# Kernel tuning notes

Hardware: AMD Instinct MI355X
Metric: run time of the kernel (lower is better)

## Reference

```python
import jax, jax.numpy as jnp
import numpy as np

N_NODES = 50000

def setup_inputs() -> dict:
    key = jax.random.key(0)
    k1, k2, k3, k4, k5 = jax.random.split(key, 5)
    x = jax.random.normal(k1, (50000, 64), dtype=jnp.float32)
    adj_rows = jax.random.randint(k2, (800000,), 0, 50000, dtype=jnp.int32)
    adj_cols = jax.random.randint(k3, (800000,), 0, 50000, dtype=jnp.int32)
    adj_vals = jax.random.uniform(k4, (800000,), dtype=jnp.float32)
    ws = jax.random.uniform(k5, (4,), dtype=jnp.float32)
    return {"x": x, "adj_rows": adj_rows, "adj_cols": adj_cols, "adj_vals": adj_vals, "ws": ws, "idx": 0}

def reference(x, adj_rows, adj_cols, adj_vals, ws, idx):
    # spmm: out[r] = sum_{e: rows[e]==r} vals[e] * x[cols[e]]
    msgs = adj_vals[:, None] * x[adj_cols]              # [E, d]
    spmm = jax.ops.segment_sum(msgs, adj_rows, num_segments=N_NODES)  # [N, d]
    return ws[idx] * spmm
```

## Files before the change

kernel.cpp:

```cpp
#include <hip/hip_runtime.h>

#define N_NODES 50000
#define N_EDGES 800000
#define D 64

#define NBUCK 782
#define CAP   2048
#define SRT_CAP 2048

#define A_EPB 4096
#define A_BLOCKS ((N_EDGES + A_EPB - 1) / A_EPB)
#define A_THREADS 512

#define F_THREADS 512

typedef unsigned short ushort_t;

__global__ __launch_bounds__(256) void cvt_kernel(
    const float* __restrict__ x, ushort_t* __restrict__ xb,
    int* __restrict__ gcur)
{
    if (blockIdx.x == 0) {
        for (int j = threadIdx.x; j < NBUCK; j += 256) gcur[j] = j * CAP;
    }
    int i = blockIdx.x * 256 + threadIdx.x;
    float4 v = reinterpret_cast<const float4*>(x)[i];
    ushort4 o;
    unsigned bx;
    bx = __float_as_uint(v.x); o.x = (ushort_t)((bx + 0x7fffu + ((bx >> 16) & 1u)) >> 16);
    bx = __float_as_uint(v.y); o.y = (ushort_t)((bx + 0x7fffu + ((bx >> 16) & 1u)) >> 16);
    bx = __float_as_uint(v.z); o.z = (ushort_t)((bx + 0x7fffu + ((bx >> 16) & 1u)) >> 16);
    bx = __float_as_uint(v.w); o.w = (ushort_t)((bx + 0x7fffu + ((bx >> 16) & 1u)) >> 16);
    reinterpret_cast<ushort4*>(xb)[i] = o;
}

__global__ __launch_bounds__(A_THREADS) void bin_kernel(
    const int* __restrict__ rows, const int* __restrict__ cols,
    const float* __restrict__ vals, int* __restrict__ gcur,
    int2* __restrict__ buckets)
{
    __shared__ int2 rec[A_EPB];
    __shared__ int2 srt[A_EPB];
    __shared__ int cnt[NBUCK];
    __shared__ int lofs[NBUCK];
    __shared__ int lcur[NBUCK];
    __shared__ int bbase[NBUCK];

    const int tid = threadIdx.x;
    const int e0  = blockIdx.x * A_EPB;
    const int n   = min(A_EPB, N_EDGES - e0);

    for (int i = tid; i < NBUCK; i += A_THREADS) cnt[i] = 0;
    __syncthreads();

    for (int i = tid; i < n; i += A_THREADS) {
        int r = rows[e0 + i];
        int c = cols[e0 + i];
        float v = vals[e0 + i];
        rec[i].x = (int)(((unsigned)r << 16) | (unsigned)c);
        rec[i].y = __float_as_int(v);
        atomicAdd(&cnt[r >> 6], 1);
    }
    __syncthreads();

    if (tid < 64) {
        int lane = tid, carry = 0;
        for (int seg = 0; seg < (NBUCK + 63) / 64; ++seg) {
            int j = seg * 64 + lane;
            int v = (j < NBUCK) ? cnt[j] : 0;
            int incl = v;
            for (int off = 1; off < 64; off <<= 1) {
                int u = __shfl_up(incl, off);
                if (lane >= off) incl += u;
            }
            if (j < NBUCK) lofs[j] = carry + incl - v;
            carry += __shfl(incl, 63);
        }
    }
    __syncthreads();

    for (int j = tid; j < NBUCK; j += A_THREADS) {
        int c = cnt[j];
        bbase[j] = c ? atomicAdd(&gcur[j], c) : 0;
        lcur[j]  = lofs[j];
    }
    __syncthreads();

    for (int i = tid; i < n; i += A_THREADS) {
        int2 rv = rec[i];
        int b = ((unsigned)rv.x) >> 22;
        int p = atomicAdd(&lcur[b], 1);
        srt[p] = rv;
    }
    __syncthreads();

    for (int i = tid; i < n; i += A_THREADS) {
        int2 rv = srt[i];
        int b = ((unsigned)rv.x) >> 22;
        buckets[bbase[b] + (i - lofs[b])] = rv;
    }
}

__global__ __launch_bounds__(F_THREADS) void sortgather_kernel(
    const ushort_t* __restrict__ xb, const int2* __restrict__ buckets,
    const int* __restrict__ gcur, const float* __restrict__ ws,
    const int* __restrict__ idx, float* __restrict__ out)
{
    __shared__ int2 srt[SRT_CAP];
    __shared__ int cnt[64];
    __shared__ int lofs[65];
    __shared__ int lcur[64];

    const int b    = blockIdx.x;
    const int tid  = threadIdx.x;
    const int lane = tid & 63;
    const int w    = tid >> 6;
    const int base = b * CAP;
    const int nb   = gcur[b] - base;

    if (tid < 64) cnt[tid] = 0;
    __syncthreads();

    for (int i = tid; i < nb; i += F_THREADS) {
        int rx = buckets[base + i].x;
        atomicAdd(&cnt[(rx >> 16) & 63], 1);
    }
    __syncthreads();

    if (w == 0) {
        int v = cnt[lane];
        int incl = v;
        for (int off = 1; off < 64; off <<= 1) {
            int u = __shfl_up(incl, off);
            if (lane >= off) incl += u;
        }
        lofs[lane] = incl - v;
        if (lane == 63) lofs[64] = incl;
    }
    __syncthreads();
    if (tid < 64) lcur[tid] = lofs[tid];
    __syncthreads();

    for (int i = tid; i < nb; i += F_THREADS) {
        int2 rv = buckets[base + i];
        int p = atomicAdd(&lcur[(rv.x >> 16) & 63], 1);
        srt[p] = make_int2((rv.x & 0xffff) << 7, rv.y);
    }
    __syncthreads();

    const float wgt = ws[idx[0]];
    const int g4       = (lane >> 5) << 2;
    const int lane_off = (lane & 31) << 2;
    const char* xbase  = (const char*)xb;

    for (int q = 0; q < 8; ++q) {
        const int lr = w * 8 + q;
        const int s0 = lofs[lr];
        const int s1 = lofs[lr + 1];
        float accL = 0.f, accH = 0.f;
        for (int cb = s0; cb < s1; cb += 32) {
            int le = cb + (lane & 31);
            int2 cv = srt[le < s1 ? le : s0];
            int offs  = cv.x;
            int vbits = (le < s1) ? cv.y : 0;
#pragma unroll
            for (int p = 0; p < 16; ++p) {
                int src = g4 + (p << 3);
                int o  = __builtin_amdgcn_ds_bpermute(src, offs);
                int vb = __builtin_amdgcn_ds_bpermute(src, vbits);
                unsigned u2 = *reinterpret_cast<const unsigned*>(
                    xbase + (unsigned)o + lane_off);
                float xlo = __uint_as_float(u2 << 16);
                float xhi = __uint_as_float(u2 & 0xffff0000u);
                float v = __int_as_float(vb);
                if (p & 1) { accH += v * xhi; accL += v * xlo; }
                else       { accL += v * xlo; accH += v * xhi; }
            }
        }
        accL += __shfl_xor(accL, 32);
        accH += __shfl_xor(accH, 32);
        const int row = b * 64 + lr;
        if (lane < 32 && row < N_NODES) {
            float2 o2 = make_float2(wgt * accL, wgt * accH);
            reinterpret_cast<float2*>(out)[(size_t)row * (D / 2) + (lane & 31)] = o2;
        }
    }
}

extern "C" void kernel_launch(void* const* d_in, const int* in_sizes, int n_in,
                              void* d_out, int out_size, void* d_ws, size_t ws_size,
                              hipStream_t stream) {
    const float* x    = (const float*)d_in[0];
    const int*   rows = (const int*)d_in[1];
    const int*   cols = (const int*)d_in[2];
    const float* vals = (const float*)d_in[3];
    const float* ws   = (const float*)d_in[4];
    const int*   idx  = (const int*)d_in[5];
    float*       out  = (float*)d_out;

    const size_t xb_bytes      = (size_t)N_NODES * D * sizeof(ushort_t);
    const size_t buckets_bytes = (size_t)NBUCK * CAP * sizeof(int2);

    char* wsb = (char*)d_ws;
    ushort_t* xb      = (ushort_t*)wsb;
    int2*     buckets = (int2*)(wsb + xb_bytes);
    int*      gcur    = (int*)(wsb + xb_bytes + buckets_bytes);

    cvt_kernel<<<dim3(N_NODES * D / 4 / 256), dim3(256), 0, stream>>>(x, xb, gcur);

    bin_kernel<<<dim3(A_BLOCKS), dim3(A_THREADS), 0, stream>>>(
        rows, cols, vals, gcur, buckets);

    sortgather_kernel<<<dim3(NBUCK), dim3(F_THREADS), 0, stream>>>(
        xb, buckets, gcur, ws, idx, out);
}
```

Baseline: 55.66 us.

## Halve bucket size to 32 rows and gather 4 features per lane with 8-byte loads

Buckets now cover 32 rows instead of 64 (1563 buckets of capacity 1024), and the gather kernel uses 256 threads. Each wavefront processes 4 edges at once, with 16 lanes each loading a ushort4 (8 bytes) of the bf16 row, then reduces across lane groups with two xor shuffles. The binning kernel drops the staging rec buffer and rereads rows/cols/vals from global memory in the scatter pass, trading more global reads for less LDS and better occupancy. The smaller capacity per bucket raises the risk of overflow if any 32-row bucket receives more than 1024 edges.

After: 52.49 us. 5.7% less time.

```diff
diff --git a/kernel.cpp b/kernel.cpp
--- a/kernel.cpp
+++ b/kernel.cpp
@@ -4,15 +4,15 @@
 #define N_EDGES 800000
 #define D 64
 
-#define NBUCK 782
-#define CAP   2048
-#define SRT_CAP 2048
+#define NBUCK 1563
+#define CAP   1024
+#define SRT_CAP 1024
 
 #define A_EPB 4096
 #define A_BLOCKS ((N_EDGES + A_EPB - 1) / A_EPB)
 #define A_THREADS 512
 
-#define F_THREADS 512
+#define F_THREADS 256
 
 typedef unsigned short ushort_t;
 
@@ -39,7 +39,6 @@
     const float* __restrict__ vals, int* __restrict__ gcur,
     int2* __restrict__ buckets)
 {
-    __shared__ int2 rec[A_EPB];
     __shared__ int2 srt[A_EPB];
     __shared__ int cnt[NBUCK];
     __shared__ int lofs[NBUCK];
@@ -53,14 +52,8 @@
     for (int i = tid; i < NBUCK; i += A_THREADS) cnt[i] = 0;
     __syncthreads();
 
-    for (int i = tid; i < n; i += A_THREADS) {
-        int r = rows[e0 + i];
-        int c = cols[e0 + i];
-        float v = vals[e0 + i];
-        rec[i].x = (int)(((unsigned)r << 16) | (unsigned)c);
-        rec[i].y = __float_as_int(v);
-        atomicAdd(&cnt[r >> 6], 1);
-    }
+    for (int i = tid; i < n; i += A_THREADS)
+        atomicAdd(&cnt[rows[e0 + i] >> 5], 1);
     __syncthreads();
 
     if (tid < 64) {
@@ -87,16 +80,18 @@
     __syncthreads();
 
     for (int i = tid; i < n; i += A_THREADS) {
-        int2 rv = rec[i];
-        int b = ((unsigned)rv.x) >> 22;
-        int p = atomicAdd(&lcur[b], 1);
-        srt[p] = rv;
+        int r = rows[e0 + i];
+        int c = cols[e0 + i];
+        float v = vals[e0 + i];
+        int p = atomicAdd(&lcur[r >> 5], 1);
+        srt[p] = make_int2((int)(((unsigned)r << 16) | (unsigned)c),
+                           __float_as_int(v));
     }
     __syncthreads();
 
     for (int i = tid; i < n; i += A_THREADS) {
         int2 rv = srt[i];
-        int b = ((unsigned)rv.x) >> 22;
+        int b = ((unsigned)rv.x) >> 21;
         buckets[bbase[b] + (i - lofs[b])] = rv;
     }
 }
@@ -107,9 +102,9 @@
     const int* __restrict__ idx, float* __restrict__ out)
 {
     __shared__ int2 srt[SRT_CAP];
-    __shared__ int cnt[64];
-    __shared__ int lofs[65];
-    __shared__ int lcur[64];
+    __shared__ int cnt[32];
+    __shared__ int lofs[33];
+    __shared__ int lcur[32];
 
     const int b    = blockIdx.x;
     const int tid  = threadIdx.x;
@@ -118,71 +113,73 @@
     const int base = b * CAP;
     const int nb   = gcur[b] - base;
 
-    if (tid < 64) cnt[tid] = 0;
+    if (tid < 32) cnt[tid] = 0;
     __syncthreads();
 
     for (int i = tid; i < nb; i += F_THREADS) {
         int rx = buckets[base + i].x;
-        atomicAdd(&cnt[(rx >> 16) & 63], 1);
-    }
-    __syncthreads();
-
-    if (w == 0) {
+        atomicAdd(&cnt[(rx >> 16) & 31], 1);
+    }
+    __syncthreads();
+
+    if (w == 0 && lane < 32) {
         int v = cnt[lane];
         int incl = v;
-        for (int off = 1; off < 64; off <<= 1) {
+        for (int off = 1; off < 32; off <<= 1) {
             int u = __shfl_up(incl, off);
             if (lane >= off) incl += u;
         }
         lofs[lane] = incl - v;
-        if (lane == 63) lofs[64] = incl;
-    }
-    __syncthreads();
-    if (tid < 64) lcur[tid] = lofs[tid];
+        if (lane == 31) lofs[32] = incl;
+    }
+    __syncthreads();
+    if (tid < 32) lcur[tid] = lofs[tid];
     __syncthreads();
 
     for (int i = tid; i < nb; i += F_THREADS) {
         int2 rv = buckets[base + i];
-        int p = atomicAdd(&lcur[(rv.x >> 16) & 63], 1);
+        int p = atomicAdd(&lcur[(rv.x >> 16) & 31], 1);
         srt[p] = make_int2((rv.x & 0xffff) << 7, rv.y);
     }
     __syncthreads();
 
-    const float wgt = ws[idx[0]];
-    const int g4       = (lane >> 5) << 2;
-    const int lane_off = (lane & 31) << 2;
-    const char* xbase  = (const char*)xb;
+    const float wgt  = ws[idx[0]];
+    const int   l15  = lane & 15;
+    const int   eo   = lane >> 4;
+    const char* xbase = (const char*)xb;
 
     for (int q = 0; q < 8; ++q) {
         const int lr = w * 8 + q;
         const int s0 = lofs[lr];
         const int s1 = lofs[lr + 1];
-        float accL = 0.f, accH = 0.f;
+        float a0 = 0.f, a1 = 0.f, a2 = 0.f, a3 = 0.f;
         for (int cb = s0; cb < s1; cb += 32) {
             int le = cb + (lane & 31);
             int2 cv = srt[le < s1 ? le : s0];
             int offs  = cv.x;
             int vbits = (le < s1) ? cv.y : 0;
 #pragma unroll
-            for (int p = 0; p < 16; ++p) {
-                int src = g4 + (p << 3);
+            for (int p = 0; p < 8; ++p) {
+                int src = ((p << 2) + eo) << 2;
                 int o  = __builtin_amdgcn_ds_bpermute(src, offs);
                 int vb = __builtin_amdgcn_ds_bpermute(src, vbits);
-                unsigned u2 = *reinterpret_cast<const unsigned*>(
-                    xbase + (unsigned)o + lane_off);
-                float xlo = __uint_as_float(u2 << 16);
-                float xhi = __uint_as_float(u2 & 0xffff0000u);
+                ushort4 u4 = *reinterpret_cast<const ushort4*>(
+                    xbase + (unsigned)o + (l15 << 3));
                 float v = __int_as_float(vb);
-                if (p & 1) { accH += v * xhi; accL += v * xlo; }
-                else       { accL += v * xlo; accH += v * xhi; }
+                a0 += v * __uint_as_float(((unsigned)u4.x) << 16);
+                a1 += v * __uint_as_float(((unsigned)u4.y) << 16);
+                a2 += v * __uint_as_float(((unsigned)u4.z) << 16);
+                a3 += v * __uint_as_float(((unsigned)u4.w) << 16);
             }
         }
-        accL += __shfl_xor(accL, 32);
-        accH += __shfl_xor(accH, 32);
-        const int row = b * 64 + lr;
-        if (lane < 32 && row < N_NODES) {
-            float2 o2 = make_float2(wgt * accL, wgt * accH);
-            reinterpret_cast<float2*>(out)[(size_t)row * (D / 2) + (lane & 31)] = o2;
+        a0 += __shfl_xor(a0, 16); a1 += __shfl_xor(a1, 16);
+        a2 += __shfl_xor(a2, 16); a3 += __shfl_xor(a3, 16);
+        a0 += __shfl_xor(a0, 32); a1 += __shfl_xor(a1, 32);
+        a2 += __shfl_xor(a2, 32); a3 += __shfl_xor(a3, 32);
+        const int row = b * 32 + lr;
+        if (lane < 16 && row < N_NODES) {
+            float4 o4 = make_float4(wgt * a0, wgt * a1, wgt * a2, wgt * a3);
+            reinterpret_cast<float4*>(out)[(size_t)row * (D / 4) + l15] = o4;
         }
     }
 }
```
